# Performance work log

Measured on AMD Instinct MI355X. Metric: run time of the kernel, lower is better.

## Reference

```python
import jax, jax.numpy as jnp
import numpy as np

C_IN = 34   # C*V = 2*17 channels after reshape
C_MID = 16
C_OUT = 3
N_LAYERS = 3
BN_EPS = 1e-5
NEG_SLOPE = 0.01


def setup_inputs() -> dict:
    key = jax.random.key(0)
    ks = jax.random.split(key, 16)
    B, C, T, V = 512, 2, 2048, 17
    s = 1.0 / np.sqrt(C_IN)
    inp = {
        "x": jax.random.normal(ks[0], (B, C, T, V), dtype=jnp.float32),
        # stacked per-layer 1x1-conv (linear) weights for Q/K/V of 3 attention layers
        "wq": jax.random.normal(ks[1], (N_LAYERS, C_IN, C_IN), dtype=jnp.float32) * s,
        "bq": jax.random.normal(ks[2], (N_LAYERS, C_IN), dtype=jnp.float32) * 0.02,
        "wk": jax.random.normal(ks[3], (N_LAYERS, C_IN, C_IN), dtype=jnp.float32) * s,
        "bk": jax.random.normal(ks[4], (N_LAYERS, C_IN), dtype=jnp.float32) * 0.02,
        "wv": jax.random.normal(ks[5], (N_LAYERS, C_IN, C_IN), dtype=jnp.float32) * s,
        "bv": jax.random.normal(ks[6], (N_LAYERS, C_IN), dtype=jnp.float32) * 0.02,
        # head: conv1 -> BN -> LeakyReLU -> conv2
        "w1": jax.random.normal(ks[7], (C_MID, C_IN), dtype=jnp.float32) * s,
        "b1": jax.random.normal(ks[8], (C_MID,), dtype=jnp.float32) * 0.02,
        "gamma": jnp.ones((C_MID,), dtype=jnp.float32),
        "beta": jnp.zeros((C_MID,), dtype=jnp.float32),
        "mean": jax.random.normal(ks[9], (C_MID,), dtype=jnp.float32) * 0.1,
        "var": jax.random.uniform(ks[10], (C_MID,), dtype=jnp.float32, minval=0.5, maxval=1.5),
        "w2": jax.random.normal(ks[11], (C_OUT, C_MID), dtype=jnp.float32) * (1.0 / np.sqrt(C_MID)),
        "b2": jax.random.normal(ks[12], (C_OUT,), dtype=jnp.float32) * 0.02,
    }
    return inp


def _conv1x1(w, b, h):
    # 1x1 Conv1d == linear over channel dim: (O,C) x (B,C,T) -> (B,O,T)
    return jnp.einsum('oc,bct->bot', w, h) + b[:, None]


def reference(x, wq, bq, wk, bk, wv, bv, w1, b1, gamma, beta, mean, var, w2, b2):
    B, C, T, V = x.shape
    h = x.transpose(0, 1, 3, 2).reshape(B, C * V, T)  # (B, 34, T)
    scale = 1.0 / (T ** 0.5)  # K.size(-1) ** 0.5 in the original
    for i in range(N_LAYERS):
        Q = _conv1x1(wq[i], bq[i], h)
        K = _conv1x1(wk[i], bk[i], h)
        Vv = _conv1x1(wv[i], bv[i], h)
        scores = jnp.einsum('bct,bdt->bcd', Q, K) * scale  # (B, 34, 34) channel attention
        attn = jax.nn.softmax(scores, axis=-1)
        h = jnp.einsum('bcd,bdt->bct', attn, Vv)
    y = _conv1x1(w1, b1, h)                               # (B, 16, T)
    inv = gamma / jnp.sqrt(var + BN_EPS)                  # inference-mode BatchNorm1d
    y = (y - mean[:, None]) * inv[:, None] + beta[:, None]
    y = jnp.where(y > 0, y, NEG_SLOPE * y)                # LeakyReLU
    return _conv1x1(w2, b2, y)                            # (B, 3, T)
```

## Files before the change

kernel.cpp:

```cpp
#include <hip/hip_runtime.h>

#define CV   34
#define TTOT 2048
#define NB   512
#define XB   69632
#define XC   34816

#define GS_STRIDE 1192
#define RB_OFF    (512 * 1192)
#define RB_STRIDE 1040

typedef __attribute__((ext_vector_type(8))) short v8s;
typedef __attribute__((ext_vector_type(4))) float v4f;

__device__ __forceinline__ unsigned short f2bf(float f) {
    unsigned int u = __float_as_uint(f);
    u = u + 0x7FFFu + ((u >> 16) & 1u);
    return (unsigned short)(u >> 16);
}
__device__ __forceinline__ float bf2f(unsigned short s) {
    return __uint_as_float(((unsigned int)s) << 16);
}

struct SmemGramA {
    unsigned short Hh[48][152];
    unsigned short Hl[48][152];
};
struct SmemGramB {
    float Gpart[4][34][36];
    float spart[4][36];
};

__global__ __launch_bounds__(256) void k_gram(const float* __restrict__ x,
                                              float* __restrict__ ws) {
    __shared__ union { SmemGramA a; SmemGramB b; } sm;

    const int b    = blockIdx.x >> 2;
    const int seg  = blockIdx.x & 3;
    const int tid  = threadIdx.x;
    const int l    = tid & 63;
    const int w    = tid >> 6;
    const int row16 = l & 15;
    const int quad  = l >> 4;
    const float* xb = x + (size_t)b * XB;

    v4f accG[3][3];
    v4f accS[3];
    v4f vz = {0.f, 0.f, 0.f, 0.f};
#pragma unroll
    for (int r = 0; r < 3; ++r) {
        accS[r] = vz;
#pragma unroll
        for (int c = 0; c < 3; ++c) accG[r][c] = vz;
    }
    v8s ones;
#pragma unroll
    for (int i = 0; i < 8; ++i) ones[i] = (short)0x3F80;

    for (int ch = 0; ch < 4; ++ch) {
        const int t0 = seg * 512 + ch * 128;
        __syncthreads();
        for (int i = tid; i < 1088; i += 256) {
            int co = (i >= 544);
            int j4 = i - co * 544;
            const float4 f4 = *(const float4*)(xb + co * XC + t0 * 17 + j4 * 4);
            const float fv[4] = {f4.x, f4.y, f4.z, f4.w};
#pragma unroll
            for (int e = 0; e < 4; ++e) {
                int j = j4 * 4 + e;
                int t = j / 17;
                int v = j - t * 17;
                float f = fv[e];
                unsigned short hb = f2bf(f);
                sm.a.Hh[co * 17 + v][t] = hb;
                sm.a.Hl[co * 17 + v][t] = f2bf(f - bf2f(hb));
            }
        }
        __syncthreads();
        const int koff = w * 32 + quad * 8;
        v8s fh[3], fl4[3];
#pragma unroll
        for (int r = 0; r < 3; ++r) {
            fh[r]  = *(const v8s*)&sm.a.Hh[r * 16 + row16][koff];
            fl4[r] = *(const v8s*)&sm.a.Hl[r * 16 + row16][koff];
        }
#pragma unroll
        for (int r = 0; r < 3; ++r) {
#pragma unroll
            for (int c = 0; c < 3; ++c) {
                accG[r][c] = __builtin_amdgcn_mfma_f32_16x16x32_bf16(fh[r],  fh[c],  accG[r][c], 0, 0, 0);
                accG[r][c] = __builtin_amdgcn_mfma_f32_16x16x32_bf16(fh[r],  fl4[c], accG[r][c], 0, 0, 0);
                accG[r][c] = __builtin_amdgcn_mfma_f32_16x16x32_bf16(fl4[r], fh[c],  accG[r][c], 0, 0, 0);
            }
            accS[r] = __builtin_amdgcn_mfma_f32_16x16x32_bf16(fh[r],  ones, accS[r], 0, 0, 0);
            accS[r] = __builtin_amdgcn_mfma_f32_16x16x32_bf16(fl4[r], ones, accS[r], 0, 0, 0);
        }
    }

    __syncthreads();
#pragma unroll
    for (int r = 0; r < 3; ++r) {
#pragma unroll
        for (int c = 0; c < 3; ++c) {
#pragma unroll
            for (int i = 0; i < 4; ++i) {
                int m = r * 16 + quad * 4 + i;
                int n = c * 16 + row16;
                if (m < 34 && n < 34) sm.b.Gpart[w][m][n] = accG[r][c][i];
            }
        }
        if (row16 == 0) {
#pragma unroll
            for (int i = 0; i < 4; ++i) {
                int m = r * 16 + quad * 4 + i;
                if (m < 34) sm.b.spart[w][m] = accS[r][i];
            }
        }
    }
    __syncthreads();
    float* gout = ws + (size_t)b * GS_STRIDE;
    for (int idx = tid; idx < 1156; idx += 256) {
        int m = idx / 34, n = idx - m * 34;
        atomicAdd(&gout[idx], sm.b.Gpart[0][m][n] + sm.b.Gpart[1][m][n] +
                              sm.b.Gpart[2][m][n] + sm.b.Gpart[3][m][n]);
    }
    if (tid < 34)
        atomicAdd(&gout[1156 + tid], sm.b.spart[0][tid] + sm.b.spart[1][tid] +
                                     sm.b.spart[2][tid] + sm.b.spart[3][tid]);
}


__device__ __forceinline__ void mm24(const float L[][36], const float R[][36],
                                     float D[][36], int u) {
    int ti = u / 9, tj = u - ti * 9;
    int i0 = ti * 2, j0 = tj * 4;
    float acc[2][4] = {};
    for (int e0 = 0; e0 < 36; e0 += 4) {
        float4 lv[2], rv[4];
        lv[0] = *(const float4*)&L[i0][e0];
        lv[1] = *(const float4*)&L[i0 + 1][e0];
#pragma unroll
        for (int c = 0; c < 4; ++c) rv[c] = *(const float4*)&R[j0 + c][e0];
#pragma unroll
        for (int a = 0; a < 2; ++a)
#pragma unroll
            for (int c = 0; c < 4; ++c)
                acc[a][c] += lv[a].x * rv[c].x + lv[a].y * rv[c].y +
                             lv[a].z * rv[c].z + lv[a].w * rv[c].w;
    }
#pragma unroll
    for (int a = 0; a < 2; ++a)
#pragma unroll
        for (int c = 0; c < 4; ++c) D[i0 + a][j0 + c] = acc[a][c];
}

__device__ __forceinline__ void mmG4(const float* __restrict__ Lg,
                                     const float R[][36], float D[][36],
                                     int transpose, int u) {
    int ti = u / 9, tj = u - ti * 9;
    int i0 = ti * 4, j0 = tj * 4;
    float acc[4][4] = {};
    for (int e0 = 0; e0 < 32; e0 += 4) {
        float2 la[4], lb[4];
        float4 rv[4];
#pragma unroll
        for (int a = 0; a < 4; ++a) {
            int ri = i0 + a; ri = ri < 34 ? ri : 33;
            la[a] = *(const float2*)(Lg + ri * 34 + e0);
            lb[a] = *(const float2*)(Lg + ri * 34 + e0 + 2);
        }
#pragma unroll
        for (int c = 0; c < 4; ++c) rv[c] = *(const float4*)&R[j0 + c][e0];
#pragma unroll
        for (int a = 0; a < 4; ++a)
#pragma unroll
            for (int c = 0; c < 4; ++c)
                acc[a][c] += la[a].x * rv[c].x + la[a].y * rv[c].y +
                             lb[a].x * rv[c].z + lb[a].y * rv[c].w;
    }
    {
        float2 la[4];
#pragma unroll
        for (int a = 0; a < 4; ++a) {
            int ri = i0 + a; ri = ri < 34 ? ri : 33;
            la[a] = *(const float2*)(Lg + ri * 34 + 32);
        }
#pragma unroll
        for (int c = 0; c < 4; ++c) {
            float r0 = R[j0 + c][32], r1 = R[j0 + c][33];
#pragma unroll
            for (int a = 0; a < 4; ++a) acc[a][c] += la[a].x * r0 + la[a].y * r1;
        }
    }
#pragma unroll
    for (int a = 0; a < 4; ++a) {
        if (i0 + a < 34) {
#pragma unroll
            for (int c = 0; c < 4; ++c) {
                if (transpose) D[j0 + c][i0 + a] = acc[a][c];
                else           D[i0 + a][j0 + c] = acc[a][c];
            }
        }
    }
}

__global__ __launch_bounds__(256) void k_chain(
    const float* __restrict__ wq, const float* __restrict__ bq,
    const float* __restrict__ wk, const float* __restrict__ bk,
    const float* __restrict__ wv, const float* __restrict__ bv,
    const float* __restrict__ w1, const float* __restrict__ b1,
    const float* __restrict__ gamma, const float* __restrict__ beta,
    const float* __restrict__ mean, const float* __restrict__ var,
    float* __restrict__ ws) {
    __shared__ float G0b[36][36], At[36][36], Aq[36][36], Ak[36][36],
        AvT[36][36], S1[36][36], Sc[36][36];
    __shared__ float s0v[36], a_[36], aq_[36], ak_[36], avv_[36],
        qs_[36], ks_[36], invv[16];

    const int tid = threadIdx.x;
    const int b   = blockIdx.x;
    const float* gsb = ws + (size_t)b * GS_STRIDE;

    for (int i = tid; i < 1296; i += 256) {
        int m = i / 36, n = i - m * 36;
        G0b[m][n] = 0; At[m][n] = 0; Aq[m][n] = 0; Ak[m][n] = 0;
        AvT[m][n] = 0; S1[m][n] = 0; Sc[m][n] = 0;
    }
    if (tid < 36) {
        s0v[tid] = 0; a_[tid] = 0; aq_[tid] = 0; ak_[tid] = 0; avv_[tid] = 0;
        qs_[tid] = 0; ks_[tid] = 0;
    }
    __syncthreads();
    for (int i = tid; i < 1156; i += 256) {
        int m = i / 34, n = i - m * 34;
        G0b[m][n] = gsb[i];
        Aq[m][n] = wq[i]; Ak[m][n] = wk[i]; AvT[n][m] = wv[i];
    }
    if (tid < 34) {
        s0v[tid] = gsb[1156 + tid];
        aq_[tid] = bq[tid]; ak_[tid] = bk[tid]; avv_[tid] = bv[tid];
    }
    __syncthreads();

    for (int lyr = 0; lyr < 3; ++lyr) {
        const float* wql = wq + lyr * 1156;
        const float* wkl = wk + lyr * 1156;
        const float* wvl = wv + lyr * 1156;
        if (lyr > 0) {
            if (tid < 243) {
                int g = tid / 81, u = tid - g * 81;
                const float* Lg = (g == 0) ? wql : (g == 1) ? wkl : wvl;
                float (*D)[36] = (g == 0) ? Aq : (g == 1) ? Ak : AvT;
                mmG4(Lg, At, D, g == 2, u);
            }
            __syncthreads();
        }
        if (tid < 153) {
            mm24(Aq, G0b, S1, tid);
        } else if (lyr > 0 && tid < 255) {
            int u = tid - 153, r = u / 34, c = u - r * 34;
            const float* wrow = ((r == 0) ? wql : (r == 1) ? wkl : wvl) + c * 34;
            float s = 0;
            for (int e = 0; e < 34; ++e) s += wrow[e] * a_[e];
            float bb = (r == 0) ? bq[lyr * 34 + c]
                     : (r == 1) ? bk[lyr * 34 + c] : bv[lyr * 34 + c];
            if (r == 0) aq_[c] = s + bb;
            else if (r == 1) ak_[c] = s + bb;
            else avv_[c] = s + bb;
        }
        __syncthreads();
        if (tid < 153) {
            mm24(S1, Ak, Sc, tid);
        } else if (tid >= 160 && tid < 228) {
            int u = tid - 160, r = u / 34, c = u - r * 34;
            const float (*M)[36] = r ? Ak : Aq;
            float s = 0;
            for (int e = 0; e < 34; ++e) s += M[c][e] * s0v[e];
            if (r == 0) qs_[c] = s; else ks_[c] = s;
        }
        __syncthreads();
        if (tid < 34) {
            const int c = tid;
            const float scale = 0.022097086912079608f;
            float mx = -1e30f;
            for (int d = 0; d < 34; ++d) {
                float v = (Sc[c][d] + qs_[c] * ak_[d] + aq_[c] * ks_[d] +
                           2048.0f * aq_[c] * ak_[d]) * scale;
                Sc[c][d] = v;
                mx = fmaxf(mx, v);
            }
            float sum = 0;
            for (int d = 0; d < 34; ++d) {
                float e = __expf(Sc[c][d] - mx);
                Sc[c][d] = e;
                sum += e;
            }
            float rs = 1.0f / sum;
            for (int d = 0; d < 34; ++d) Sc[c][d] *= rs;
        }
        __syncthreads();
        if (tid < 153) {
            mm24(AvT, Sc, At, tid);
        } else if (tid >= 160 && tid < 194) {
            int c = tid - 160;
            float s = 0;
            for (int d = 0; d < 34; ++d) s += Sc[c][d] * avv_[d];
            a_[c] = s;
        }
        __syncthreads();
    }

    if (tid < 72) {
        int ti = tid / 9, tj = tid - ti * 9;
        int i0 = ti * 2, j0 = tj * 4;
        float acc[2][4] = {};
        for (int e0 = 0; e0 < 32; e0 += 4) {
            float2 la[2], lb[2];
            float4 rv[4];
#pragma unroll
            for (int a = 0; a < 2; ++a) {
                la[a] = *(const float2*)(w1 + (i0 + a) * 34 + e0);
                lb[a] = *(const float2*)(w1 + (i0 + a) * 34 + e0 + 2);
            }
#pragma unroll
            for (int c = 0; c < 4; ++c) rv[c] = *(const float4*)&At[j0 + c][e0];
#pragma unroll
            for (int a = 0; a < 2; ++a)
#pragma unroll
                for (int c = 0; c < 4; ++c)
                    acc[a][c] += la[a].x * rv[c].x + la[a].y * rv[c].y +
                                 lb[a].x * rv[c].z + lb[a].y * rv[c].w;
        }
        {
            float2 la[2];
#pragma unroll
            for (int a = 0; a < 2; ++a)
                la[a] = *(const float2*)(w1 + (i0 + a) * 34 + 32);
#pragma unroll
            for (int c = 0; c < 4; ++c) {
                float r0 = At[j0 + c][32], r1 = At[j0 + c][33];
#pragma unroll
                for (int a = 0; a < 2; ++a) acc[a][c] += la[a].x * r0 + la[a].y * r1;
            }
        }
#pragma unroll
        for (int a = 0; a < 2; ++a)
#pragma unroll
            for (int c = 0; c < 4; ++c) S1[i0 + a][j0 + c] = acc[a][c];
    } else if (tid < 88) {
        int o = tid - 72;
        invv[o] = gamma[o] * rsqrtf(var[o] + 1e-5f);
    } else if (tid < 104) {
        int o = tid - 88;
        float s = 0;
        for (int e = 0; e < 34; ++e) s += w1[o * 34 + e] * a_[e];
        ks_[o] = s + b1[o];
    }
    __syncthreads();
    float* wb = ws + RB_OFF + (size_t)b * RB_STRIDE;
    if (tid < 16)
        wb[1024 + tid] = (ks_[tid] - mean[tid]) * invv[tid] + beta[tid];
    unsigned short* wp = (unsigned short*)wb;
    for (int i = tid; i < 1024; i += 256) {
        int o = i >> 6, c = i & 63;
        float vv = (c < 34) ? S1[o][c] * invv[o] : 0.0f;
        unsigned short hb = f2bf(vv);
        wp[i] = hb;
        wp[1024 + i] = f2bf(vv - bf2f(hb));
    }
}

__global__ __launch_bounds__(256) void k_out(const float* __restrict__ x,
                                             const float* __restrict__ w2,
                                             const float* __restrict__ b2,
                                             const float* __restrict__ ws,
                                             float* __restrict__ out) {
    __shared__ unsigned short HtH[128][72];
    __shared__ unsigned short HtL[128][72];

    const int tid  = threadIdx.x;
    const int b    = blockIdx.x >> 3;
    const int seg  = (blockIdx.x & 7) * 256;
    const int l    = tid & 63;
    const int w    = tid >> 6;
    const int quad = l >> 4;
    const int col  = l & 15;

    const float* wb = ws + RB_OFF + (size_t)b * RB_STRIDE;
    const unsigned short* wp = (const unsigned short*)wb;
    v8s aH[2], aL[2];
#pragma unroll
    for (int ks = 0; ks < 2; ++ks) {
        aH[ks] = *(const v8s*)&wp[col * 64 + ks * 32 + quad * 8];
        aL[ks] = *(const v8s*)&wp[1024 + col * 64 + ks * 32 + quad * 8];
    }
    float cyr[4], w2r[3][4];
#pragma unroll
    for (int i = 0; i < 4; ++i) {
        int o = quad * 4 + i;
        cyr[i] = wb[1024 + o];
#pragma unroll
        for (int p = 0; p < 3; ++p) w2r[p][i] = w2[p * 16 + o];
    }
    float b2r[3] = {b2[0], b2[1], b2[2]};
    const float* xb = x + (size_t)b * XB;

    for (int idx = tid; idx < 128 * 30; idx += 256) {
        int t = idx / 30;
        int c = 34 + (idx - t * 30);
        HtH[t][c] = 0;
        HtL[t][c] = 0;
    }

    for (int ch = 0; ch < 2; ++ch) {
        const int t0c = seg + ch * 128;
        __syncthreads();
        for (int i = tid; i < 1088; i += 256) {
            int co = (i >= 544);
            int j4 = i - co * 544;
            const float4 f4 = *(const float4*)(xb + co * XC + t0c * 17 + j4 * 4);
            const float fv[4] = {f4.x, f4.y, f4.z, f4.w};
#pragma unroll
            for (int e = 0; e < 4; ++e) {
                int j = j4 * 4 + e;
                int t = j / 17;
                int v = j - t * 17;
                float f = fv[e];
                unsigned short hb = f2bf(f);
                HtH[t][co * 17 + v] = hb;
                HtL[t][co * 17 + v] = f2bf(f - bf2f(hb));
            }
        }
        __syncthreads();
        for (int tt = w; tt < 8; tt += 4) {
            const int tBase = tt * 16;
            v4f acc = {0.f, 0.f, 0.f, 0.f};
#pragma unroll
            for (int ks = 0; ks < 2; ++ks) {
                v8s bH = *(const v8s*)&HtH[tBase + col][ks * 32 + quad * 8];
                v8s bL = *(const v8s*)&HtL[tBase + col][ks * 32 + quad * 8];
                acc = __builtin_amdgcn_mfma_f32_16x16x32_bf16(aH[ks], bH, acc, 0, 0, 0);
                acc = __builtin_amdgcn_mfma_f32_16x16x32_bf16(aH[ks], bL, acc, 0, 0, 0);
                acc = __builtin_amdgcn_mfma_f32_16x16x32_bf16(aL[ks], bH, acc, 0, 0, 0);
            }
            float op[3] = {0, 0, 0};
#pragma unroll
            for (int i = 0; i < 4; ++i) {
                float y = acc[i] + cyr[i];
                float z = (y > 0.f) ? y : 0.01f * y;
#pragma unroll
                for (int p = 0; p < 3; ++p) op[p] += w2r[p][i] * z;
            }
#pragma unroll
            for (int p = 0; p < 3; ++p) {
                op[p] += __shfl_xor(op[p], 16);
                op[p] += __shfl_xor(op[p], 32);
            }
            if (l < 16) {
                int tg = t0c + tBase + l;
#pragma unroll
                for (int p = 0; p < 3; ++p)
                    out[((size_t)b * 3 + p) * 2048 + tg] = op[p] + b2r[p];
            }
        }
    }
}

extern "C" void kernel_launch(void* const* d_in, const int* in_sizes, int n_in,
                              void* d_out, int out_size, void* d_ws, size_t ws_size,
                              hipStream_t stream) {
    const float* x     = (const float*)d_in[0];
    const float* wq    = (const float*)d_in[1];
    const float* bq    = (const float*)d_in[2];
    const float* wk    = (const float*)d_in[3];
    const float* bk    = (const float*)d_in[4];
    const float* wv    = (const float*)d_in[5];
    const float* bv    = (const float*)d_in[6];
    const float* w1    = (const float*)d_in[7];
    const float* b1    = (const float*)d_in[8];
    const float* gamma = (const float*)d_in[9];
    const float* beta  = (const float*)d_in[10];
    const float* mean  = (const float*)d_in[11];
    const float* var   = (const float*)d_in[12];
    const float* w2    = (const float*)d_in[13];
    const float* b2    = (const float*)d_in[14];
    float* ws  = (float*)d_ws;
    float* out = (float*)d_out;

    hipMemsetAsync(d_ws, 0, (size_t)NB * GS_STRIDE * sizeof(float), stream);
    k_gram<<<dim3(2048), dim3(256), 0, stream>>>(x, ws);
    k_chain<<<dim3(512), dim3(256), 0, stream>>>(wq, bq, wk, bk, wv, bv,
                                                 w1, b1, gamma, beta, mean, var, ws);
    k_out<<<dim3(4096), dim3(256), 0, stream>>>(x, w2, b2, ws, out);
}
```

Measured before the change: 334.1 us.

## Stage raw x via async global-to-LDS loads with double buffering, split bf16 at fragment load

Both the Gram and output kernels now copy raw fp32 chunks of x straight into LDS with global_load_lds into double buffers, so the next chunk loads while the current one is computed. The hi/lo bf16 split now happens when MFMA fragments are read, using packed cvt instructions, instead of during staging. The output kernel drops the zero-padded second K-step: channels 32 and 33 are added as scalar FMAs, which halves the packed weight buffer. Occupancy hints are added to the launch bounds. The risks are strided LDS reads (stride 17) that may cause bank conflicts, and more VALU work per fragment.

```diff
diff --git a/kernel.cpp b/kernel.cpp
--- a/kernel.cpp
+++ b/kernel.cpp
@@ -8,7 +8,7 @@
 
 #define GS_STRIDE 1192
 #define RB_OFF    (512 * 1192)
-#define RB_STRIDE 1040
+#define RB_STRIDE 576
 
 typedef __attribute__((ext_vector_type(8))) short v8s;
 typedef __attribute__((ext_vector_type(4))) float v4f;
@@ -22,18 +22,55 @@
     return __uint_as_float(((unsigned int)s) << 16);
 }
 
-struct SmemGramA {
-    unsigned short Hh[48][152];
-    unsigned short Hl[48][152];
-};
+__device__ __forceinline__ unsigned int cvtpk_bf16(float a, float b) {
+    unsigned int r;
+    asm("v_cvt_pk_bf16_f32 %0, %1, %2" : "=v"(r) : "v"(a), "v"(b));
+    return r;
+}
+
+__device__ __forceinline__ void split8(const float (&f)[8], v8s* hi, v8s* lo) {
+    union { unsigned int u[4]; v8s s; } H, L;
+#pragma unroll
+    for (int p = 0; p < 4; ++p) {
+        float a = f[2 * p], b = f[2 * p + 1];
+        unsigned int h = cvtpk_bf16(a, b);
+        float ra = a - __uint_as_float(h << 16);
+        float rb = b - __uint_as_float(h & 0xFFFF0000u);
+        L.u[p] = cvtpk_bf16(ra, rb);
+        H.u[p] = h;
+    }
+    *hi = H.s;
+    *lo = L.s;
+}
+
+__device__ __forceinline__ void stage_chunk(const float* __restrict__ xb, int t0,
+                                            float* rawbuf, int w, int lane) {
+#pragma unroll
+    for (int i = 0; i < 5; ++i) {
+        int idx = i * 4 + w;
+        if (idx < 17) {
+            int fl = idx * 256 + lane * 4;
+            int co = (fl >= 2176) ? 1 : 0;
+            const float* g = xb + t0 * 17 + fl + co * 32640;
+            __builtin_amdgcn_global_load_lds(
+                (const __attribute__((address_space(1))) void*)g,
+                (__attribute__((address_space(3))) void*)(rawbuf + idx * 256),
+                16, 0, 0);
+        }
+    }
+}
+
 struct SmemGramB {
     float Gpart[4][34][36];
     float spart[4][36];
 };
 
-__global__ __launch_bounds__(256) void k_gram(const float* __restrict__ x,
-                                              float* __restrict__ ws) {
-    __shared__ union { SmemGramA a; SmemGramB b; } sm;
+__global__ __launch_bounds__(256, 4) void k_gram(const float* __restrict__ x,
+                                                 float* __restrict__ ws) {
+    __shared__ __align__(16) union {
+        float raw[2][4352];
+        SmemGramB b;
+    } sm;
 
     const int b    = blockIdx.x >> 2;
     const int seg  = blockIdx.x & 3;
@@ -43,6 +80,16 @@
     const int row16 = l & 15;
     const int quad  = l >> 4;
     const float* xb = x + (size_t)b * XB;
+    const int t0 = seg * 512;
+
+    int offc[3];
+#pragma unroll
+    for (int r = 0; r < 3; ++r) {
+        int c = r * 16 + row16;
+        if (c > 33) c = 33;
+        offc[r] = (c >= 17) ? (2159 + c) : c;
+    }
+    const int koff = w * 32 + quad * 8;
 
     v4f accG[3][3];
     v4f accS[3];
@@ -57,32 +104,22 @@
 #pragma unroll
     for (int i = 0; i < 8; ++i) ones[i] = (short)0x3F80;
 
+    stage_chunk(xb, t0, sm.raw[0], w, l);
+    __syncthreads();
+
     for (int ch = 0; ch < 4; ++ch) {
-        const int t0 = seg * 512 + ch * 128;
-        __syncthreads();
-        for (int i = tid; i < 1088; i += 256) {
-            int co = (i >= 544);
-            int j4 = i - co * 544;
-            const float4 f4 = *(const float4*)(xb + co * XC + t0 * 17 + j4 * 4);
-            const float fv[4] = {f4.x, f4.y, f4.z, f4.w};
-#pragma unroll
-            for (int e = 0; e < 4; ++e) {
-                int j = j4 * 4 + e;
-                int t = j / 17;
-                int v = j - t * 17;
-                float f = fv[e];
-                unsigned short hb = f2bf(f);
-                sm.a.Hh[co * 17 + v][t] = hb;
-                sm.a.Hl[co * 17 + v][t] = f2bf(f - bf2f(hb));
-            }
-        }
-        __syncthreads();
-        const int koff = w * 32 + quad * 8;
+        const int cur = ch & 1;
+        if (ch < 3) stage_chunk(xb, t0 + (ch + 1) * 128, sm.raw[cur ^ 1], w, l);
+
+        const float* rb = sm.raw[cur] + koff * 17;
         v8s fh[3], fl4[3];
 #pragma unroll
         for (int r = 0; r < 3; ++r) {
-            fh[r]  = *(const v8s*)&sm.a.Hh[r * 16 + row16][koff];
-            fl4[r] = *(const v8s*)&sm.a.Hl[r * 16 + row16][koff];
+            const float* p = rb + offc[r];
+            float f[8];
+#pragma unroll
+            for (int e = 0; e < 8; ++e) f[e] = p[e * 17];
+            split8(f, &fh[r], &fl4[r]);
         }
 #pragma unroll
         for (int r = 0; r < 3; ++r) {
@@ -95,9 +132,9 @@
             accS[r] = __builtin_amdgcn_mfma_f32_16x16x32_bf16(fh[r],  ones, accS[r], 0, 0, 0);
             accS[r] = __builtin_amdgcn_mfma_f32_16x16x32_bf16(fl4[r], ones, accS[r], 0, 0, 0);
         }
-    }
-
-    __syncthreads();
+        __syncthreads();
+    }
+
 #pragma unroll
     for (int r = 0; r < 3; ++r) {
 #pragma unroll
@@ -358,25 +395,28 @@
     }
     __syncthreads();
     float* wb = ws + RB_OFF + (size_t)b * RB_STRIDE;
-    if (tid < 16)
-        wb[1024 + tid] = (ks_[tid] - mean[tid]) * invv[tid] + beta[tid];
+    if (tid < 16) {
+        wb[512 + tid] = (ks_[tid] - mean[tid]) * invv[tid] + beta[tid];
+    } else if (tid < 48) {
+        int u = tid - 16, o = u & 15, cc = u >> 4;
+        wb[528 + cc * 16 + o] = S1[o][32 + cc] * invv[o];
+    }
     unsigned short* wp = (unsigned short*)wb;
-    for (int i = tid; i < 1024; i += 256) {
-        int o = i >> 6, c = i & 63;
-        float vv = (c < 34) ? S1[o][c] * invv[o] : 0.0f;
+    for (int i = tid; i < 512; i += 256) {
+        int o = i >> 5, c = i & 31;
+        float vv = S1[o][c] * invv[o];
         unsigned short hb = f2bf(vv);
         wp[i] = hb;
-        wp[1024 + i] = f2bf(vv - bf2f(hb));
-    }
-}
-
-__global__ __launch_bounds__(256) void k_out(const float* __restrict__ x,
-                                             const float* __restrict__ w2,
-                                             const float* __restrict__ b2,
-                                             const float* __restrict__ ws,
-                                             float* __restrict__ out) {
-    __shared__ unsigned short HtH[128][72];
-    __shared__ unsigned short HtL[128][72];
+        wp[512 + i] = f2bf(vv - bf2f(hb));
+    }
+}
+
+__global__ __launch_bounds__(256, 4) void k_out(const float* __restrict__ x,
+                                                const float* __restrict__ w2,
+                                                const float* __restrict__ b2,
+                                                const float* __restrict__ ws,
+                                                float* __restrict__ out) {
+    __shared__ __align__(16) float raw[2][4352];
 
     const int tid  = threadIdx.x;
     const int b    = blockIdx.x >> 3;
@@ -388,65 +428,51 @@
 
     const float* wb = ws + RB_OFF + (size_t)b * RB_STRIDE;
     const unsigned short* wp = (const unsigned short*)wb;
-    v8s aH[2], aL[2];
-#pragma unroll
-    for (int ks = 0; ks < 2; ++ks) {
-        aH[ks] = *(const v8s*)&wp[col * 64 + ks * 32 + quad * 8];
-        aL[ks] = *(const v8s*)&wp[1024 + col * 64 + ks * 32 + quad * 8];
-    }
-    float cyr[4], w2r[3][4];
+    v8s aH = *(const v8s*)&wp[col * 32 + quad * 8];
+    v8s aL = *(const v8s*)&wp[512 + col * 32 + quad * 8];
+    float cyr[4], w2r[3][4], wy32r[4], wy33r[4];
 #pragma unroll
     for (int i = 0; i < 4; ++i) {
         int o = quad * 4 + i;
-        cyr[i] = wb[1024 + o];
+        cyr[i]   = wb[512 + o];
+        wy32r[i] = wb[528 + o];
+        wy33r[i] = wb[544 + o];
 #pragma unroll
         for (int p = 0; p < 3; ++p) w2r[p][i] = w2[p * 16 + o];
     }
     float b2r[3] = {b2[0], b2[1], b2[2]};
     const float* xb = x + (size_t)b * XB;
 
-    for (int idx = tid; idx < 128 * 30; idx += 256) {
-        int t = idx / 30;
-        int c = 34 + (idx - t * 30);
-        HtH[t][c] = 0;
-        HtL[t][c] = 0;
-    }
+    int offq[8];
+#pragma unroll
+    for (int e = 0; e < 8; ++e) {
+        int c = quad * 8 + e;
+        offq[e] = (c >= 17) ? (2159 + c) : c;
+    }
+
+    stage_chunk(xb, seg, raw[0], w, l);
+    __syncthreads();
 
     for (int ch = 0; ch < 2; ++ch) {
-        const int t0c = seg + ch * 128;
-        __syncthreads();
-        for (int i = tid; i < 1088; i += 256) {
-            int co = (i >= 544);
-            int j4 = i - co * 544;
-            const float4 f4 = *(const float4*)(xb + co * XC + t0c * 17 + j4 * 4);
-            const float fv[4] = {f4.x, f4.y, f4.z, f4.w};
-#pragma unroll
-            for (int e = 0; e < 4; ++e) {
-                int j = j4 * 4 + e;
-                int t = j / 17;
-                int v = j - t * 17;
-                float f = fv[e];
-                unsigned short hb = f2bf(f);
-                HtH[t][co * 17 + v] = hb;
-                HtL[t][co * 17 + v] = f2bf(f - bf2f(hb));
-            }
-        }
-        __syncthreads();
+        if (ch == 0) stage_chunk(xb, seg + 128, raw[1], w, l);
         for (int tt = w; tt < 8; tt += 4) {
-            const int tBase = tt * 16;
+            const int tl = tt * 16 + col;
+            const float* rbt = raw[ch] + tl * 17;
+            float f[8];
+#pragma unroll
+            for (int e = 0; e < 8; ++e) f[e] = rbt[offq[e]];
+            v8s bH, bL;
+            split8(f, &bH, &bL);
             v4f acc = {0.f, 0.f, 0.f, 0.f};
-#pragma unroll
-            for (int ks = 0; ks < 2; ++ks) {
-                v8s bH = *(const v8s*)&HtH[tBase + col][ks * 32 + quad * 8];
-                v8s bL = *(const v8s*)&HtL[tBase + col][ks * 32 + quad * 8];
-                acc = __builtin_amdgcn_mfma_f32_16x16x32_bf16(aH[ks], bH, acc, 0, 0, 0);
-                acc = __builtin_amdgcn_mfma_f32_16x16x32_bf16(aH[ks], bL, acc, 0, 0, 0);
-                acc = __builtin_amdgcn_mfma_f32_16x16x32_bf16(aL[ks], bH, acc, 0, 0, 0);
-            }
+            acc = __builtin_amdgcn_mfma_f32_16x16x32_bf16(aH, bH, acc, 0, 0, 0);
+            acc = __builtin_amdgcn_mfma_f32_16x16x32_bf16(aH, bL, acc, 0, 0, 0);
+            acc = __builtin_amdgcn_mfma_f32_16x16x32_bf16(aL, bH, acc, 0, 0, 0);
+            float h32 = rbt[2191];
+            float h33 = rbt[2192];
             float op[3] = {0, 0, 0};
 #pragma unroll
             for (int i = 0; i < 4; ++i) {
-                float y = acc[i] + cyr[i];
+                float y = acc[i] + cyr[i] + wy32r[i] * h32 + wy33r[i] * h33;
                 float z = (y > 0.f) ? y : 0.01f * y;
 #pragma unroll
                 for (int p = 0; p < 3; ++p) op[p] += w2r[p][i] * z;
@@ -457,12 +483,13 @@
                 op[p] += __shfl_xor(op[p], 32);
             }
             if (l < 16) {
-                int tg = t0c + tBase + l;
+                int tg = seg + ch * 128 + tt * 16 + l;
 #pragma unroll
                 for (int p = 0; p < 3; ++p)
                     out[((size_t)b * 3 + p) * 2048 + tg] = op[p] + b2r[p];
             }
         }
+        __syncthreads();
     }
 }
 
```

Result: faster. 312.2 us (-6.6%).
